# Kernel optimization log

Measured on AMD Instinct MI355X. Metric: run time of the kernel, lower is better.

## Reference

```python
import jax, jax.numpy as jnp
import numpy as np

NUM_CLASS = 20
STRIDE = 4.0
B, H, W, G, NV = 8, 128, 128, 64, 40


def setup_inputs() -> dict:
    key = jax.random.key(0)
    ks = jax.random.split(key, 8)
    keypoints = jax.random.normal(ks[0], (B, H, W, NUM_CLASS), jnp.float32)
    preg = jax.random.uniform(ks[1], (B, H, W, 4), jnp.float32, 1.0, 40.0)
    fpn = jax.random.normal(ks[2], (B, H, W, NUM_CLASS), jnp.float32)
    masks = jnp.ones((B, H, W, G), jnp.float32)
    scalar_y = jax.random.uniform(ks[3], (B, G), jnp.float32, 5.0, 25.0)
    scalar_x = jax.random.uniform(ks[4], (B, G), jnp.float32, 5.0, 25.0)
    # ground truth: [cy, cx, y1, x1, y2, x2, class]; rows >= NV are zero padding
    rng = np.random.default_rng(0)
    gt = np.zeros((B, G, 7), np.float32)
    cy = rng.uniform(20.0, 492.0, (B, NV)).astype(np.float32)
    cx = rng.uniform(20.0, 492.0, (B, NV)).astype(np.float32)
    hh = rng.uniform(16.0, 120.0, (B, NV)).astype(np.float32)
    ww = rng.uniform(16.0, 120.0, (B, NV)).astype(np.float32)
    gt[:, :NV, 0] = cy
    gt[:, :NV, 1] = cx
    gt[:, :NV, 2] = np.clip(cy - hh / 2, 1.0, 510.0)
    gt[:, :NV, 3] = np.clip(cx - ww / 2, 1.0, 510.0)
    gt[:, :NV, 4] = np.clip(cy + hh / 2, 1.0, 510.0)
    gt[:, :NV, 5] = np.clip(cx + ww / 2, 1.0, 510.0)
    gt[:, :NV, 6] = rng.integers(1, NUM_CLASS + 1, (B, NV)).astype(np.float32)
    return {
        "keypoints": keypoints,
        "preg": preg,
        "fpn": fpn,
        "ground_truth": jnp.asarray(gt),
        "masks": masks,
        "scalar_y": scalar_y,
        "scalar_x": scalar_x,
    }


def _image_loss(gravity_pred, dist_pred, heatmap_pred, gt, masks, sy, sx):
    f32 = jnp.float32
    Hh, Ww, C = gravity_pred.shape
    Gg = gt.shape[0]
    # padding boundary: first row whose cy (col 0) is the minimum (==0 padding)
    slice_index = jnp.argmin(gt[:, 0])
    valid = jnp.arange(Gg) < slice_index
    vf = valid.astype(f32)

    gy = (gt[:, 0] + 0.5) / STRIDE
    gx = (gt[:, 1] + 0.5) / STRIDE
    by1 = (gt[:, 2] + 0.5) / STRIDE
    bx1 = (gt[:, 3] + 0.5) / STRIDE
    by2 = (gt[:, 4] + 0.5) / STRIDE
    bx2 = (gt[:, 5] + 0.5) / STRIDE
    cid = gt[:, 6].astype(jnp.int32) - 1
    kp_y = jnp.clip(jnp.floor(gt[:, 0] / STRIDE).astype(jnp.int32), 0, Hh - 1)
    kp_x = jnp.clip(jnp.floor(gt[:, 1] / STRIDE).astype(jnp.int32), 0, Ww - 1)

    grid_y = (jnp.arange(Hh, dtype=f32) + 0.5)[:, None, None]  # [H,1,1]
    grid_x = (jnp.arange(Ww, dtype=f32) + 0.5)[None, :, None]  # [1,W,1]

    dist_l = grid_x - bx1  # [1,W,G]
    dist_r = bx2 - grid_x
    dist_t = grid_y - by1  # [H,1,G]
    dist_b = by2 - grid_y
    ymask = (dist_t > 0.0).astype(f32) * (dist_b > 0.0).astype(f32)
    xmask = (dist_l > 0.0).astype(f32) * (dist_r > 0.0).astype(f32)
    heatmask = ymask * xmask * masks * vf  # [H,W,G]
    dist_l = dist_l * heatmask
    dist_r = dist_r * heatmask
    dist_t = dist_t * heatmask
    dist_b = dist_b * heatmask
    loc = jnp.max(heatmask, axis=-1)  # [H,W]
    dist_area = (dist_l + dist_r) * (dist_t + dist_b)
    area_pad = dist_area + (1.0 - heatmask) * 1e8
    area_min = jnp.min(area_pad, axis=-1, keepdims=True)
    dist_mask = (dist_area == area_min).astype(f32) * loc[..., None]  # [H,W,G]
    dl = jnp.max(dist_l * dist_mask, axis=-1)
    dr = jnp.max(dist_r * dist_mask, axis=-1)
    dt = jnp.max(dist_t * dist_mask, axis=-1)
    db = jnp.max(dist_b * dist_mask, axis=-1)

    pl, pr, pt, pb = (dist_pred[..., k] for k in range(4))
    inter = (jnp.minimum(dl, pl) + jnp.minimum(dr, pr)) * (jnp.minimum(dt, pt) + jnp.minimum(db, pb))
    union = (dl + dr) * (dt + db) + (pl + pr) * (pt + pb) - inter
    iou = inter / (union + 1e-12)

    red = jnp.exp(-(((grid_y - 0.5 - jnp.floor(gy)) / jnp.sqrt(sy)) ** 2
                    + ((grid_x - 0.5 - jnp.floor(gx)) / jnp.sqrt(sx)) ** 2) / 2.0) * vf  # [H,W,G]
    iou_red = jnp.max(red, axis=-1)
    iou_loss = jnp.sum(-jnp.log(iou + 1e-12) * loc * (iou_red * 4.0 + 1.0))

    # per-class max over gts of that class (== boolean_mask + reduce_max; empty -> 0)
    seg = jnp.where(valid & (cid >= 0) & (cid < C), cid, C)
    red_gt = jnp.maximum(jax.ops.segment_max(red.transpose(2, 0, 1), seg, num_segments=C + 1)[:C], 0.0).transpose(1, 2, 0)
    hm_gt = jnp.maximum(jax.ops.segment_max(dist_mask.transpose(2, 0, 1), seg, num_segments=C + 1)[:C], 0.0).transpose(1, 2, 0)
    gt_kp = jnp.zeros((Hh, Ww, C + 1), f32).at[kp_y, kp_x, seg].max(vf)[..., :C]

    sig, ls = jax.nn.sigmoid, jax.nn.log_sigmoid
    pos = -(1.0 - sig(gravity_pred)) ** 2 * ls(gravity_pred) * gt_kp
    neg = -(1.0 - red_gt) ** 4 * sig(gravity_pred) ** 2 * (-gravity_pred + ls(gravity_pred)) * (1.0 - gt_kp)
    gravity_loss = jnp.sum(pos) + jnp.sum(neg)

    hpos = -10.0 * (1.0 - sig(heatmap_pred)) ** 2 * ls(heatmap_pred) * hm_gt
    hneg = -10.0 * sig(heatmap_pred) ** 2 * (-heatmap_pred + ls(heatmap_pred)) * (1.0 - hm_gt)
    s_hg = jnp.sum(hm_gt)
    hm_loss = jnp.sum(hneg) / (jnp.asarray(Hh * Ww * C, f32) - s_hg)

    cond = s_hg != 0.0
    safe_hg = jnp.where(cond, s_hg, 1.0)
    s_loc = jnp.sum(loc)
    safe_loc = jnp.where(s_loc > 0.0, s_loc, 1.0)
    n_valid = jnp.maximum(slice_index.astype(f32), 1.0)
    hm2 = hm_loss + jnp.sum(hpos) / safe_hg
    iou_out = jnp.where(cond, iou_loss / safe_loc, 0.0)
    grav_out = jnp.where(cond, gravity_loss / n_valid, 0.0)
    hm_out = jnp.where(cond, hm2, hm_loss)
    total = jnp.where(cond, iou_out + grav_out + hm2, hm_loss)
    return iou_out, hm_out, grav_out, total


def reference(keypoints, preg, fpn, ground_truth, masks, scalar_y, scalar_x):
    losses = jax.vmap(_image_loss)(keypoints, preg, fpn, ground_truth, masks, scalar_y, scalar_x)
    # layer returns the mean total loss over the batch
    return jnp.mean(losses[3])
```

## Files before the change

### kernel.cpp

```cpp
#include <hip/hip_runtime.h>
#include <math.h>

#define Bc 8
#define Hc 128
#define Wc 128
#define Cc 20
#define Gc 64
#define HWc (Hc*Wc)

#define WS_STRIDE 768
#define WS_NV   704
#define WS_ACC  705
#define WS_SLICE 711

__global__ __launch_bounds__(64) void prep_kernel(
    const float* __restrict__ gt, const float* __restrict__ sy,
    const float* __restrict__ sx, float* __restrict__ ws)
{
  const int b = blockIdx.x;
  const int g = threadIdx.x;
  __shared__ float cy_s[Gc];
  __shared__ int slice_s;
  const float* row = gt + (size_t)(b*Gc + g)*7;
  const float cy = row[0];
  const float cx = row[1];
  cy_s[g] = cy;
  __syncthreads();
  if (g == 0) {
    float mn = cy_s[0]; int idx = 0;
    for (int i = 1; i < Gc; ++i) { float v = cy_s[i]; if (v < mn) { mn = v; idx = i; } }
    slice_s = idx;
  }
  __syncthreads();
  const int slice = slice_s;
  float* wb = ws + (size_t)b*WS_STRIDE;
  int*  wbi = (int*)wb;
  wb[0*Gc+g] = (row[2]+0.5f)*0.25f;
  wb[1*Gc+g] = (row[3]+0.5f)*0.25f;
  wb[2*Gc+g] = (row[4]+0.5f)*0.25f;
  wb[3*Gc+g] = (row[5]+0.5f)*0.25f;
  wb[4*Gc+g] = floorf((cy+0.5f)*0.25f);
  wb[5*Gc+g] = floorf((cx+0.5f)*0.25f);
  wb[6*Gc+g] = 1.0f / sy[b*Gc+g];
  wb[7*Gc+g] = 1.0f / sx[b*Gc+g];
  const float vf = (g < slice) ? 1.0f : 0.0f;
  wb[8*Gc+g] = vf;
  const int cid = (int)row[6] - 1;
  wbi[9*Gc+g] = (vf > 0.0f && cid >= 0 && cid < Cc) ? cid : Cc;
  int kpy = (int)floorf(cy*0.25f); kpy = kpy < 0 ? 0 : (kpy > Hc-1 ? Hc-1 : kpy);
  int kpx = (int)floorf(cx*0.25f); kpx = kpx < 0 ? 0 : (kpx > Wc-1 ? Wc-1 : kpx);
  wbi[10*Gc+g] = kpy*Wc + kpx;
  if (g == 0) { wb[WS_NV] = fmaxf((float)slice, 1.0f); wbi[WS_SLICE] = slice; }
  if (g < 6) wb[WS_ACC+g] = 0.0f;
}

__device__ __forceinline__ float logsig(float x) {
  return fminf(x, 0.0f) - log1pf(__expf(-fabsf(x)));
}
__device__ __forceinline__ float sigmoidf_(float x) {
  return 1.0f / (1.0f + __expf(-x));
}
__device__ __forceinline__ float wave_sum(float v) {
  #pragma unroll
  for (int o = 32; o > 0; o >>= 1) v += __shfl_down(v, o, 64);
  return v;
}

__global__ __launch_bounds__(256) void main_kernel(
  const float* __restrict__ kpt, const float* __restrict__ preg,
  const float* __restrict__ fpn, const float* __restrict__ masks,
  float* __restrict__ ws)
{
  __shared__ float s_pg[704];
  __shared__ float s_rmax[256*21];
  __shared__ float s_part[4][6];

  const int tid = threadIdx.x;
  const int b   = blockIdx.x >> 6;
  const int pix = blockIdx.x*256 + tid;
  const int hw  = pix & (HWc-1);
  const int h = hw >> 7, w = hw & (Wc-1);

  float* wb = ws + (size_t)b*WS_STRIDE;
  { const int* src = (const int*)wb; int* dst = (int*)s_pg;
    for (int i = tid; i < 704; i += 256) dst[i] = src[i]; }
  float* rme = s_rmax + tid*21;
  #pragma unroll
  for (int c = 0; c < 21; ++c) rme[c] = 0.0f;
  __syncthreads();

  const float* s_by1 = s_pg;
  const float* s_bx1 = s_pg + 64;
  const float* s_by2 = s_pg + 128;
  const float* s_bx2 = s_pg + 192;
  const float* s_fgy = s_pg + 256;
  const float* s_fgx = s_pg + 320;
  const float* s_isy = s_pg + 384;
  const float* s_isx = s_pg + 448;
  const int*   s_seg = (const int*)(s_pg + 576);
  const int*   s_kpx = (const int*)(s_pg + 640);
  const int nslice = ((const int*)wb)[WS_SLICE];

  const float wx = w + 0.5f, hy = h + 0.5f;
  const float px_ = (float)w, py_ = (float)h;
  const float* mrow = masks + (size_t)pix * Gc;

  float amin = 3.0e38f; int gmin = -1;
  float loc = 0.0f, iou_red = 0.0f;
  unsigned kpmask = 0;

  for (int g0 = 0; g0 < nslice; g0 += 4) {
    const float4 m4 = *(const float4*)(mrow + g0);
    #pragma unroll
    for (int j = 0; j < 4; ++j) {
      const int g = g0 + j;
      if (g >= nslice) break;
      const float m = (j==0) ? m4.x : (j==1) ? m4.y : (j==2) ? m4.z : m4.w;
      const float dl = wx - s_bx1[g], dr = s_bx2[g] - wx;
      const float dt = hy - s_by1[g], db = s_by2[g] - hy;
      const bool inbox = (dl > 0.0f) & (dr > 0.0f) & (dt > 0.0f) & (db > 0.0f);
      const float hm = inbox ? m : 0.0f;
      const float area = (dl*hm + dr*hm) * (dt*hm + db*hm);
      const float ap = area + (1.0f - hm)*1e8f;
      if (ap < amin) { amin = ap; gmin = g; }
      loc = fmaxf(loc, hm);
      const float dy = py_ - s_fgy[g], dx = px_ - s_fgx[g];
      const float red = __expf(-0.5f*(dy*dy*s_isy[g] + dx*dx*s_isx[g]));
      iou_red = fmaxf(iou_red, red);
      const int c = s_seg[g];
      if (c < Cc) {
        if (red > rme[c]) rme[c] = red;
        if (s_kpx[g] == hw) kpmask |= (1u << c);
      }
    }
  }

  float dlm=0.0f, drm=0.0f, dtm=0.0f, dbm=0.0f; int cmin = Cc; float hmval = 0.0f;
  if (loc > 0.0f && gmin >= 0) {
    const float m = mrow[gmin];
    const float dl = wx - s_bx1[gmin], dr = s_bx2[gmin] - wx;
    const float dt = hy - s_by1[gmin], db = s_by2[gmin] - hy;
    dlm = dl*m*loc; drm = dr*m*loc; dtm = dt*m*loc; dbm = db*m*loc;
    cmin = s_seg[gmin];
    hmval = loc;
  }

  const float4 p4 = *(const float4*)(preg + (size_t)pix*4);
  const float inter = (fminf(dlm,p4.x)+fminf(drm,p4.y)) * (fminf(dtm,p4.z)+fminf(dbm,p4.w));
  const float uni = (dlm+drm)*(dtm+dbm) + (p4.x+p4.y)*(p4.z+p4.w) - inter;
  const float iou = inter / (uni + 1e-12f);
  const float t_iou = -logf(iou + 1e-12f) * loc * (iou_red*4.0f + 1.0f);

  float grav = 0.0f, hpos = 0.0f, hneg = 0.0f, shg = 0.0f;
  const float* kq = kpt + (size_t)pix*Cc;
  const float* fq = fpn + (size_t)pix*Cc;
  #pragma unroll
  for (int c = 0; c < Cc; ++c) {
    const float x   = kq[c];
    const float s   = sigmoidf_(x);
    const float lsx = logsig(x);
    const float rmax = rme[c];
    const float kpv  = ((kpmask >> c) & 1u) ? 1.0f : 0.0f;
    const float om  = 1.0f - rmax;
    const float om4 = (om*om)*(om*om);
    const float oms = 1.0f - s;
    const float pos_t = -(oms*oms)*lsx;
    const float neg_t = -om4*(s*s)*(lsx - x);
    grav += pos_t*kpv + neg_t*(1.0f - kpv);

    const float fx  = fq[c];
    const float sf  = sigmoidf_(fx);
    const float lsf = logsig(fx);
    const float hg  = (c == cmin) ? hmval : 0.0f;
    const float osf = 1.0f - sf;
    hpos += -10.0f*(osf*osf)*lsf*hg;
    hneg += -10.0f*(sf*sf)*(lsf - fx)*(1.0f - hg);
    shg  += hg;
  }

  float v0 = wave_sum(t_iou);
  float v1 = wave_sum(loc);
  float v2 = wave_sum(grav);
  float v3 = wave_sum(hpos);
  float v4 = wave_sum(hneg);
  float v5 = wave_sum(shg);
  const int wv = tid >> 6, ln = tid & 63;
  if (ln == 0) {
    s_part[wv][0]=v0; s_part[wv][1]=v1; s_part[wv][2]=v2;
    s_part[wv][3]=v3; s_part[wv][4]=v4; s_part[wv][5]=v5;
  }
  __syncthreads();
  if (tid < 6) {
    const float a = s_part[0][tid] + s_part[1][tid] + s_part[2][tid] + s_part[3][tid];
    atomicAdd(wb + WS_ACC + tid, a);
  }
}

__global__ __launch_bounds__(64) void fin_kernel(const float* __restrict__ ws,
                                                 float* __restrict__ out)
{
  const int b = threadIdx.x;
  float total = 0.0f;
  if (b < Bc) {
    const float* wb = ws + (size_t)b*WS_STRIDE;
    const float iou_loss = wb[WS_ACC+0];
    const float s_loc    = wb[WS_ACC+1];
    const float grav     = wb[WS_ACC+2];
    const float hposs    = wb[WS_ACC+3];
    const float hnegs    = wb[WS_ACC+4];
    const float shg      = wb[WS_ACC+5];
    const float nv       = wb[WS_NV];
    const float hm_loss  = hnegs / ((float)(HWc*Cc) - shg);
    const bool  cond     = (shg != 0.0f);
    const float safe_hg  = cond ? shg : 1.0f;
    const float safe_loc = (s_loc > 0.0f) ? s_loc : 1.0f;
    const float hm2      = hm_loss + hposs/safe_hg;
    total = cond ? (iou_loss/safe_loc + grav/nv + hm2) : hm_loss;
  }
  #pragma unroll
  for (int o = 4; o > 0; o >>= 1) total += __shfl_down(total, o, 64);
  if (b == 0) out[0] = total * (1.0f/(float)Bc);
}

extern "C" void kernel_launch(void* const* d_in, const int* in_sizes, int n_in,
                              void* d_out, int out_size, void* d_ws, size_t ws_size,
                              hipStream_t stream) {
  const float* kpt  = (const float*)d_in[0];
  const float* preg = (const float*)d_in[1];
  const float* fpn  = (const float*)d_in[2];
  const float* gt   = (const float*)d_in[3];
  const float* mk   = (const float*)d_in[4];
  const float* sy   = (const float*)d_in[5];
  const float* sx   = (const float*)d_in[6];
  float* ws  = (float*)d_ws;
  float* out = (float*)d_out;

  prep_kernel<<<Bc, 64, 0, stream>>>(gt, sy, sx, ws);
  main_kernel<<<(Bc*HWc)/256, 256, 0, stream>>>(kpt, preg, fpn, mk, ws);
  fin_kernel<<<1, 64, 0, stream>>>(ws, out);
}
```

Measured before the change: 127.9 us.

## Bucket GT objects by class to drop per-thread shared rmax array

The prep kernel now sorts valid ground-truth entries by class using counting offsets, so the main kernel can compute each class's gaussian max in a per-class loop held in registers. This removes the large 256x21 shared-memory array that capped occupancy. The main kernel also reads box and gaussian parameters straight from global memory as float4 instead of staging them in shared memory, and loads the kpt/fpn rows as float4. It rewrites sigmoid/logsigmoid to share a single exp, and computes hpos only for the one matched class. The risks are more global and L1 traffic and changed tie-breaking for the argmin box.

```diff
diff --git a/kernel.cpp b/kernel.cpp
--- a/kernel.cpp
+++ b/kernel.cpp
@@ -7,11 +7,17 @@
 #define Cc 20
 #define Gc 64
 #define HWc (Hc*Wc)
+#define NBLK (Bc*HWc/256)
 
 #define WS_STRIDE 768
-#define WS_NV   704
-#define WS_ACC  705
-#define WS_SLICE 711
+#define OFF_BOX   0
+#define OFF_RED   256
+#define OFF_KPIX  512
+#define OFF_SEG   576
+#define OFF_START 640
+#define WS_NV     704
+#define WS_ACC    705
+#define WS_SLICE  712
 
 __global__ __launch_bounds__(64) void prep_kernel(
     const float* __restrict__ gt, const float* __restrict__ sy,
@@ -19,47 +25,60 @@
 {
   const int b = blockIdx.x;
   const int g = threadIdx.x;
-  __shared__ float cy_s[Gc];
-  __shared__ int slice_s;
   const float* row = gt + (size_t)(b*Gc + g)*7;
   const float cy = row[0];
   const float cx = row[1];
-  cy_s[g] = cy;
+
+  float v = cy; int idx = g;
+  #pragma unroll
+  for (int o = 32; o > 0; o >>= 1) {
+    const float ov = __shfl_down(v, o, 64);
+    const int   oi = __shfl_down(idx, o, 64);
+    if (ov < v || (ov == v && oi < idx)) { v = ov; idx = oi; }
+  }
+  const int slice = __shfl(idx, 0, 64);
+  const bool valid = g < slice;
+  const int cid = (int)row[6] - 1;
+  const int cls = (cid >= 0 && cid < Cc) ? cid : Cc;
+
+  __shared__ int counts[Cc+1], offs[Cc+1], starts[Cc+2];
+  if (g < Cc+1) { counts[g] = 0; offs[g] = 0; }
+  __syncthreads();
+  if (valid) atomicAdd(&counts[cls], 1);
   __syncthreads();
   if (g == 0) {
-    float mn = cy_s[0]; int idx = 0;
-    for (int i = 1; i < Gc; ++i) { float v = cy_s[i]; if (v < mn) { mn = v; idx = i; } }
-    slice_s = idx;
-  }
-  __syncthreads();
-  const int slice = slice_s;
+    int acc = 0;
+    for (int c = 0; c < Cc+1; ++c) { starts[c] = acc; acc += counts[c]; }
+    starts[Cc+1] = acc;
+  }
+  __syncthreads();
+
   float* wb = ws + (size_t)b*WS_STRIDE;
   int*  wbi = (int*)wb;
-  wb[0*Gc+g] = (row[2]+0.5f)*0.25f;
-  wb[1*Gc+g] = (row[3]+0.5f)*0.25f;
-  wb[2*Gc+g] = (row[4]+0.5f)*0.25f;
-  wb[3*Gc+g] = (row[5]+0.5f)*0.25f;
-  wb[4*Gc+g] = floorf((cy+0.5f)*0.25f);
-  wb[5*Gc+g] = floorf((cx+0.5f)*0.25f);
-  wb[6*Gc+g] = 1.0f / sy[b*Gc+g];
-  wb[7*Gc+g] = 1.0f / sx[b*Gc+g];
-  const float vf = (g < slice) ? 1.0f : 0.0f;
-  wb[8*Gc+g] = vf;
-  const int cid = (int)row[6] - 1;
-  wbi[9*Gc+g] = (vf > 0.0f && cid >= 0 && cid < Cc) ? cid : Cc;
-  int kpy = (int)floorf(cy*0.25f); kpy = kpy < 0 ? 0 : (kpy > Hc-1 ? Hc-1 : kpy);
-  int kpx = (int)floorf(cx*0.25f); kpx = kpx < 0 ? 0 : (kpx > Wc-1 ? Wc-1 : kpx);
-  wbi[10*Gc+g] = kpy*Wc + kpx;
+  float4 bx;
+  bx.x = (row[2]+0.5f)*0.25f;
+  bx.y = (row[3]+0.5f)*0.25f;
+  bx.z = (row[4]+0.5f)*0.25f;
+  bx.w = (row[5]+0.5f)*0.25f;
+  ((float4*)(wb + OFF_BOX))[g] = bx;
+  wbi[OFF_SEG+g] = (valid && cls < Cc) ? cls : Cc;
+  if (valid) {
+    const int pos = starts[cls] + atomicAdd(&offs[cls], 1);
+    float4 rp;
+    rp.x = floorf((cy+0.5f)*0.25f);
+    rp.y = floorf((cx+0.5f)*0.25f);
+    rp.z = 1.0f / sy[b*Gc+g];
+    rp.w = 1.0f / sx[b*Gc+g];
+    ((float4*)(wb + OFF_RED))[pos] = rp;
+    int kpy = (int)floorf(cy*0.25f); kpy = kpy < 0 ? 0 : (kpy > Hc-1 ? Hc-1 : kpy);
+    int kpx = (int)floorf(cx*0.25f); kpx = kpx < 0 ? 0 : (kpx > Wc-1 ? Wc-1 : kpx);
+    wbi[OFF_KPIX+pos] = kpy*Wc + kpx;
+  }
+  if (g < Cc+2) wbi[OFF_START+g] = starts[g];
   if (g == 0) { wb[WS_NV] = fmaxf((float)slice, 1.0f); wbi[WS_SLICE] = slice; }
   if (g < 6) wb[WS_ACC+g] = 0.0f;
 }
 
-__device__ __forceinline__ float logsig(float x) {
-  return fminf(x, 0.0f) - log1pf(__expf(-fabsf(x)));
-}
-__device__ __forceinline__ float sigmoidf_(float x) {
-  return 1.0f / (1.0f + __expf(-x));
-}
 __device__ __forceinline__ float wave_sum(float v) {
   #pragma unroll
   for (int o = 32; o > 0; o >>= 1) v += __shfl_down(v, o, 64);
@@ -69,10 +88,8 @@
 __global__ __launch_bounds__(256) void main_kernel(
   const float* __restrict__ kpt, const float* __restrict__ preg,
   const float* __restrict__ fpn, const float* __restrict__ masks,
-  float* __restrict__ ws)
+  const float* __restrict__ wsc, float* __restrict__ wsa)
 {
-  __shared__ float s_pg[704];
-  __shared__ float s_rmax[256*21];
   __shared__ float s_part[4][6];
 
   const int tid = threadIdx.x;
@@ -81,101 +98,129 @@
   const int hw  = pix & (HWc-1);
   const int h = hw >> 7, w = hw & (Wc-1);
 
-  float* wb = ws + (size_t)b*WS_STRIDE;
-  { const int* src = (const int*)wb; int* dst = (int*)s_pg;
-    for (int i = tid; i < 704; i += 256) dst[i] = src[i]; }
-  float* rme = s_rmax + tid*21;
-  #pragma unroll
-  for (int c = 0; c < 21; ++c) rme[c] = 0.0f;
-  __syncthreads();
-
-  const float* s_by1 = s_pg;
-  const float* s_bx1 = s_pg + 64;
-  const float* s_by2 = s_pg + 128;
-  const float* s_bx2 = s_pg + 192;
-  const float* s_fgy = s_pg + 256;
-  const float* s_fgx = s_pg + 320;
-  const float* s_isy = s_pg + 384;
-  const float* s_isx = s_pg + 448;
-  const int*   s_seg = (const int*)(s_pg + 576);
-  const int*   s_kpx = (const int*)(s_pg + 640);
-  const int nslice = ((const int*)wb)[WS_SLICE];
+  const float* wb  = wsc + (size_t)b*WS_STRIDE;
+  const int*   wbi = (const int*)wb;
+  const float4* __restrict__ box4 = (const float4*)(wb + OFF_BOX);
+  const float4* __restrict__ red4 = (const float4*)(wb + OFF_RED);
+  const int nslice = wbi[WS_SLICE];
 
   const float wx = w + 0.5f, hy = h + 0.5f;
   const float px_ = (float)w, py_ = (float)h;
-  const float* mrow = masks + (size_t)pix * Gc;
-
-  float amin = 3.0e38f; int gmin = -1;
-  float loc = 0.0f, iou_red = 0.0f;
-  unsigned kpmask = 0;
-
-  for (int g0 = 0; g0 < nslice; g0 += 4) {
-    const float4 m4 = *(const float4*)(mrow + g0);
+  const float4* mrow4 = (const float4*)(masks + (size_t)pix*Gc);
+  const float4 p4 = *(const float4*)(preg + (size_t)pix*4);
+
+  float amin = 3.0e38f; float loc = 0.0f; int gmin = 0;
+  #pragma unroll
+  for (int g0 = 0; g0 < Gc; g0 += 4) {
+    float4 m4 = make_float4(0.f, 0.f, 0.f, 0.f);
+    if (g0 < nslice) m4 = mrow4[g0 >> 2];
     #pragma unroll
     for (int j = 0; j < 4; ++j) {
       const int g = g0 + j;
-      if (g >= nslice) break;
       const float m = (j==0) ? m4.x : (j==1) ? m4.y : (j==2) ? m4.z : m4.w;
-      const float dl = wx - s_bx1[g], dr = s_bx2[g] - wx;
-      const float dt = hy - s_by1[g], db = s_by2[g] - hy;
-      const bool inbox = (dl > 0.0f) & (dr > 0.0f) & (dt > 0.0f) & (db > 0.0f);
-      const float hm = inbox ? m : 0.0f;
+      const float4 bx = box4[g];
+      const float dl = wx - bx.y, dr = bx.w - wx;
+      const float dt = hy - bx.x, db = bx.z - hy;
+      const bool inb = (dl > 0.f) & (dr > 0.f) & (dt > 0.f) & (db > 0.f) && (g < nslice);
+      const float hm = inb ? m : 0.f;
       const float area = (dl*hm + dr*hm) * (dt*hm + db*hm);
-      const float ap = area + (1.0f - hm)*1e8f;
+      const float ap = area + (1.f - hm)*1e8f;
       if (ap < amin) { amin = ap; gmin = g; }
       loc = fmaxf(loc, hm);
-      const float dy = py_ - s_fgy[g], dx = px_ - s_fgx[g];
-      const float red = __expf(-0.5f*(dy*dy*s_isy[g] + dx*dx*s_isx[g]));
+    }
+  }
+
+  const float4* kq4 = (const float4*)(kpt + (size_t)pix*Cc);
+  const float4* fq4 = (const float4*)(fpn + (size_t)pix*Cc);
+  float kf[Cc], ff[Cc];
+  #pragma unroll
+  for (int t = 0; t < 5; ++t) {
+    const float4 a = kq4[t], c = fq4[t];
+    kf[4*t]=a.x; kf[4*t+1]=a.y; kf[4*t+2]=a.z; kf[4*t+3]=a.w;
+    ff[4*t]=c.x; ff[4*t+1]=c.y; ff[4*t+2]=c.z; ff[4*t+3]=c.w;
+  }
+
+  float dlm=0.f, drm=0.f, dtm=0.f, dbm=0.f, hmval=0.f; int cmin = Cc;
+  if (loc > 0.f) {
+    const float m = masks[(size_t)pix*Gc + gmin];
+    const float4 bx = box4[gmin];
+    const float dl = wx - bx.y, dr = bx.w - wx;
+    const float dt = hy - bx.x, db = bx.z - hy;
+    const float area = (dl*m + dr*m) * (dt*m + db*m);
+    if (area == amin) {
+      dlm = dl*m*loc; drm = dr*m*loc; dtm = dt*m*loc; dbm = db*m*loc;
+      cmin = wbi[OFF_SEG + gmin];
+      hmval = loc;
+    }
+  }
+
+  float iou_red = 0.f, grav = 0.f, hneg = 0.f;
+  int s0 = wbi[OFF_START];
+  #pragma unroll
+  for (int c = 0; c < Cc; ++c) {
+    const int s1 = wbi[OFF_START + c + 1];
+    float rmax = 0.f; bool kpv = false;
+    for (int i = s0; i < s1; ++i) {
+      const float4 rp = red4[i];
+      const int kpix = wbi[OFF_KPIX + i];
+      const float dy = py_ - rp.x, dx = px_ - rp.y;
+      const float red = __expf(-0.5f*(dy*dy*rp.z + dx*dx*rp.w));
       iou_red = fmaxf(iou_red, red);
-      const int c = s_seg[g];
-      if (c < Cc) {
-        if (red > rme[c]) rme[c] = red;
-        if (s_kpx[g] == hw) kpmask |= (1u << c);
-      }
-    }
-  }
-
-  float dlm=0.0f, drm=0.0f, dtm=0.0f, dbm=0.0f; int cmin = Cc; float hmval = 0.0f;
-  if (loc > 0.0f && gmin >= 0) {
-    const float m = mrow[gmin];
-    const float dl = wx - s_bx1[gmin], dr = s_bx2[gmin] - wx;
-    const float dt = hy - s_by1[gmin], db = s_by2[gmin] - hy;
-    dlm = dl*m*loc; drm = dr*m*loc; dtm = dt*m*loc; dbm = db*m*loc;
-    cmin = s_seg[gmin];
-    hmval = loc;
-  }
-
-  const float4 p4 = *(const float4*)(preg + (size_t)pix*4);
+      rmax = fmaxf(rmax, red);
+      kpv = kpv | (kpix == hw);
+    }
+    s0 = s1;
+    const float x  = kf[c];
+    const float e  = __expf(-fabsf(x));
+    const float t  = 1.f + e;
+    const float r  = 1.f / t;
+    const float L  = __logf(t);
+    const float s  = (x >= 0.f) ? r : e*r;
+    const float lsx = fminf(x, 0.f) - L;
+    const float kv = kpv ? 1.f : 0.f;
+    const float om = 1.f - rmax;
+    const float om4 = (om*om)*(om*om);
+    const float oms = 1.f - s;
+    grav += (-(oms*oms)*lsx)*kv + (-om4*(s*s)*(lsx - x))*(1.f - kv);
+
+    const float fx  = ff[c];
+    const float ef  = __expf(-fabsf(fx));
+    const float tf  = 1.f + ef;
+    const float rf  = 1.f / tf;
+    const float Lf  = __logf(tf);
+    const float sf  = (fx >= 0.f) ? rf : ef*rf;
+    const float lsf = fminf(fx, 0.f) - Lf;
+    hneg += -10.f*(sf*sf)*(lsf - fx);
+  }
+  {
+    const int e20 = wbi[OFF_START + Cc + 1];
+    for (int i = s0; i < e20; ++i) {
+      const float4 rp = red4[i];
+      const float dy = py_ - rp.x, dx = px_ - rp.y;
+      iou_red = fmaxf(iou_red, __expf(-0.5f*(dy*dy*rp.z + dx*dx*rp.w)));
+    }
+  }
+
   const float inter = (fminf(dlm,p4.x)+fminf(drm,p4.y)) * (fminf(dtm,p4.z)+fminf(dbm,p4.w));
   const float uni = (dlm+drm)*(dtm+dbm) + (p4.x+p4.y)*(p4.z+p4.w) - inter;
   const float iou = inter / (uni + 1e-12f);
-  const float t_iou = -logf(iou + 1e-12f) * loc * (iou_red*4.0f + 1.0f);
-
-  float grav = 0.0f, hpos = 0.0f, hneg = 0.0f, shg = 0.0f;
-  const float* kq = kpt + (size_t)pix*Cc;
-  const float* fq = fpn + (size_t)pix*Cc;
-  #pragma unroll
-  for (int c = 0; c < Cc; ++c) {
-    const float x   = kq[c];
-    const float s   = sigmoidf_(x);
-    const float lsx = logsig(x);
-    const float rmax = rme[c];
-    const float kpv  = ((kpmask >> c) & 1u) ? 1.0f : 0.0f;
-    const float om  = 1.0f - rmax;
-    const float om4 = (om*om)*(om*om);
-    const float oms = 1.0f - s;
-    const float pos_t = -(oms*oms)*lsx;
-    const float neg_t = -om4*(s*s)*(lsx - x);
-    grav += pos_t*kpv + neg_t*(1.0f - kpv);
-
-    const float fx  = fq[c];
-    const float sf  = sigmoidf_(fx);
-    const float lsf = logsig(fx);
-    const float hg  = (c == cmin) ? hmval : 0.0f;
-    const float osf = 1.0f - sf;
-    hpos += -10.0f*(osf*osf)*lsf*hg;
-    hneg += -10.0f*(sf*sf)*(lsf - fx)*(1.0f - hg);
-    shg  += hg;
+  const float t_iou = -__logf(iou + 1e-12f) * loc * (iou_red*4.f + 1.f);
+
+  float hpos = 0.f, shg = 0.f;
+  if (hmval > 0.f && cmin < Cc) {
+    float fx = 0.f;
+    #pragma unroll
+    for (int c = 0; c < Cc; ++c) if (c == cmin) fx = ff[c];
+    const float ef  = __expf(-fabsf(fx));
+    const float tf  = 1.f + ef;
+    const float rf  = 1.f / tf;
+    const float Lf  = __logf(tf);
+    const float sf  = (fx >= 0.f) ? rf : ef*rf;
+    const float lsf = fminf(fx, 0.f) - Lf;
+    const float osf = 1.f - sf;
+    hpos = -10.f*(osf*osf)*lsf*hmval;
+    hneg -= (-10.f*(sf*sf)*(lsf - fx))*hmval;
+    shg = hmval;
   }
 
   float v0 = wave_sum(t_iou);
@@ -192,7 +237,7 @@
   __syncthreads();
   if (tid < 6) {
     const float a = s_part[0][tid] + s_part[1][tid] + s_part[2][tid] + s_part[3][tid];
-    atomicAdd(wb + WS_ACC + tid, a);
+    atomicAdd(wsa + (size_t)b*WS_STRIDE + WS_ACC + tid, a);
   }
 }
 
@@ -236,6 +281,6 @@
   float* out = (float*)d_out;
 
   prep_kernel<<<Bc, 64, 0, stream>>>(gt, sy, sx, ws);
-  main_kernel<<<(Bc*HWc)/256, 256, 0, stream>>>(kpt, preg, fpn, mk, ws);
+  main_kernel<<<NBLK, 256, 0, stream>>>(kpt, preg, fpn, mk, ws, ws);
   fin_kernel<<<1, 64, 0, stream>>>(ws, out);
 }
```

Result: slower. 138.1 us (+7.9%).
